# Performance work log

Measured on AMD Instinct MI355X. Metric: run time of the kernel, lower is better.

Reference implementation:

```python
import jax, jax.numpy as jnp
import numpy as np

N, E, G = 100000, 800000, 64
F_IN, H = 92, 4
D1, D2, D3 = 32, 64, 128  # per-head out dims: hidden//2, hidden, 2*hidden
HID, LAT = 64, 128
FINAL = H * D3  # 512
NEG_SLOPE = 0.2


def _p(key, shape, scale=0.05):
    return jax.random.normal(key, shape, dtype=jnp.float32) * scale


def setup_inputs() -> dict:
    key = jax.random.key(0)
    ks = jax.random.split(key, 32)
    node_feat = jax.random.normal(ks[0], (N, F_IN), dtype=jnp.float32)
    src = jax.random.randint(ks[1], (E,), 0, N)
    dst = jax.random.randint(ks[2], (E,), 0, N)
    graph_id = jnp.sort(jax.random.randint(ks[3], (N,), 0, G))
    d = {"node_feat": node_feat, "src": src, "dst": dst, "graph_id": graph_id}
    # GAT layer params (DGL GATConv: fc no bias, attn_l/attn_r [H,D], bias [H*D])
    dims = [(F_IN, D1), (H * D1, D2), (H * D2, D3)]
    i = 4
    for li, (fi, do) in enumerate(dims, 1):
        d[f"W{li}"] = _p(ks[i], (fi, H * do)); i += 1
        d[f"al{li}"] = _p(ks[i], (H, do)); i += 1
        d[f"ar{li}"] = _p(ks[i], (H, do)); i += 1
        d[f"b{li}"] = jnp.zeros((H * do,), dtype=jnp.float32)
    # gate MLP: Linear(final, hid) -> ReLU -> Linear(hid, 1)
    d["Wg1"] = _p(ks[i], (FINAL, HID)); i += 1
    d["bg1"] = jnp.zeros((HID,), dtype=jnp.float32)
    d["Wg2"] = _p(ks[i], (HID, 1)); i += 1
    d["bg2"] = jnp.zeros((1,), dtype=jnp.float32)
    d["Wmu"] = _p(ks[i], (FINAL, LAT)); i += 1
    d["bmu"] = jnp.zeros((LAT,), dtype=jnp.float32)
    d["Wlv"] = _p(ks[i], (FINAL, LAT)); i += 1
    d["blv"] = jnp.zeros((LAT,), dtype=jnp.float32)
    return d


def gat_layer(h, W, al, ar, b, src, dst, heads, d_out):
    n = h.shape[0]
    Wh = (h @ W).reshape(n, heads, d_out)                      # [N,H,D]
    el = jnp.einsum('nhd,hd->nh', Wh, al)                      # a_l . Wh
    er = jnp.einsum('nhd,hd->nh', Wh, ar)
    e = jax.nn.leaky_relu(el[src] + er[dst], NEG_SLOPE)        # [E,H]
    m = jax.ops.segment_max(e, dst, num_segments=n)
    m = jnp.where(jnp.isfinite(m), m, 0.0)                     # zero-in-degree guard
    ex = jnp.exp(e - m[dst])
    s = jax.ops.segment_sum(ex, dst, num_segments=n)
    a = ex / jnp.maximum(s[dst], 1e-9)                         # edge softmax
    msg = a[:, :, None] * Wh[src]                              # [E,H,D] (peak intermediate)
    out = jax.ops.segment_sum(msg, dst, num_segments=n)        # scatter-aggregate
    out = out + b.reshape(1, heads, d_out)
    return out.reshape(n, heads * d_out)                       # flatten(1)


def attention_pool(h, graph_id, Wg1, bg1, Wg2, bg2, num_graphs):
    gate = jax.nn.relu(h @ Wg1 + bg1) @ Wg2 + bg2              # [N,1]
    m = jax.ops.segment_max(gate, graph_id, num_segments=num_graphs)
    ex = jnp.exp(gate - m[graph_id])
    s = jax.ops.segment_sum(ex, graph_id, num_segments=num_graphs)
    a = ex / jnp.maximum(s[graph_id], 1e-9)                    # softmax over nodes per graph
    return jax.ops.segment_sum(a * h, graph_id, num_segments=num_graphs)  # [G,final]


def reference(node_feat, src, dst, graph_id,
              W1, al1, ar1, b1, W2, al2, ar2, b2, W3, al3, ar3, b3,
              Wg1, bg1, Wg2, bg2, Wmu, bmu, Wlv, blv):
    h = jax.nn.elu(gat_layer(node_feat, W1, al1, ar1, b1, src, dst, H, D1))
    h = jax.nn.elu(gat_layer(h, W2, al2, ar2, b2, src, dst, H, D2))
    h = jax.nn.elu(gat_layer(h, W3, al3, ar3, b3, src, dst, H, D3))
    g = attention_pool(h, graph_id, Wg1, bg1, Wg2, bg2, G)
    mu = g @ Wmu + bmu
    logvar = g @ Wlv + blv
    return (mu, logvar)
```

## Files before the change

kernel.cpp:

```cpp
#include <hip/hip_runtime.h>
#include <math.h>

#define NNODES 100000
#define NEDGES 800000
#define NGRAPH 64
#define NHEAD  4
#define FINALD 512
#define HIDG   64
#define LATD   128
#define K1P    96
#define NB_SCAN 98
#define PQ     16

typedef unsigned int uint;
typedef unsigned short ushort;
typedef __attribute__((ext_vector_type(8))) short bf16x8;
typedef __attribute__((ext_vector_type(4))) float f32x4;

__device__ __forceinline__ float bflo(uint u) { return __uint_as_float(u << 16); }
__device__ __forceinline__ float bfhi(uint u) { return __uint_as_float(u & 0xffff0000u); }
__device__ __forceinline__ ushort f2bf(float f) {
    uint u = __float_as_uint(f);
    return (ushort)((u + 0x7fffu + ((u >> 16) & 1u)) >> 16);
}
__device__ __forceinline__ uint pack2(float a, float b) {
    return (uint)f2bf(a) | ((uint)f2bf(b) << 16);
}

__device__ __forceinline__ void async_copy16(const ushort* gsrc, ushort* lds_base) {
    __builtin_amdgcn_global_load_lds(
        (const __attribute__((address_space(1))) uint*)gsrc,
        (__attribute__((address_space(3))) uint*)lds_base,
        16, 0, 0);
}

__global__ void init_kernel(int* __restrict__ deg, const int* __restrict__ gid,
                            int* __restrict__ gstart) {
    int i = blockIdx.x * blockDim.x + threadIdx.x;
    if (i < NNODES) deg[i] = 0;
    if (i <= NGRAPH) {
        int lo = 0, hi = NNODES;
        while (lo < hi) {
            int mid = (lo + hi) >> 1;
            if (gid[mid] < i) lo = mid + 1; else hi = mid;
        }
        gstart[i] = lo;
    }
}
__global__ void count_kernel(const int* __restrict__ dst, int* __restrict__ deg) {
    int e = blockIdx.x * blockDim.x + threadIdx.x;
    if (e < NEDGES) atomicAdd(&deg[dst[e]], 1);
}
__global__ __launch_bounds__(1024) void scan_block_kernel(const int* __restrict__ deg,
                                                          int* __restrict__ off,
                                                          int* __restrict__ bsum) {
    __shared__ int buf[1024];
    int t = threadIdx.x;
    int i = blockIdx.x * 1024 + t;
    int x = (i < NNODES) ? deg[i] : 0;
    buf[t] = x;
    __syncthreads();
    for (int s = 1; s < 1024; s <<= 1) {
        int v = (t >= s) ? buf[t - s] : 0;
        __syncthreads();
        buf[t] += v;
        __syncthreads();
    }
    if (i < NNODES) off[i] = buf[t] - x;
    if (t == 1023) bsum[blockIdx.x] = buf[1023];
}
__global__ __launch_bounds__(128) void scan_bsum_kernel(int* __restrict__ bsum) {
    __shared__ int buf[128];
    int t = threadIdx.x;
    int x = (t < NB_SCAN) ? bsum[t] : 0;
    buf[t] = x;
    __syncthreads();
    for (int s = 1; s < 128; s <<= 1) {
        int v = (t >= s) ? buf[t - s] : 0;
        __syncthreads();
        buf[t] += v;
        __syncthreads();
    }
    if (t < NB_SCAN) bsum[t] = buf[t] - x;
    if (t == 0) bsum[NB_SCAN] = buf[NB_SCAN - 1];
}
__global__ __launch_bounds__(1024) void scan_add_kernel(int* __restrict__ off,
                                                        const int* __restrict__ bsum,
                                                        int* __restrict__ cursor) {
    int i = blockIdx.x * 1024 + threadIdx.x;
    if (i < NNODES) {
        int v = off[i] + bsum[blockIdx.x];
        off[i] = v;
        cursor[i] = v;
    }
    if (i == 0) off[NNODES] = bsum[NB_SCAN];
}
__global__ void scatter_kernel(const int* __restrict__ src, const int* __restrict__ dst,
                               int* __restrict__ cursor, int* __restrict__ src_csr) {
    int e = blockIdx.x * blockDim.x + threadIdx.x;
    if (e >= NEDGES) return;
    int p = atomicAdd(&cursor[dst[e]], 1);
    src_csr[p] = src[e];
}

#define C1 (128 * K1P)
#define C2 (256 * 128)
#define C3 (512 * 256)
#define CG (64 * 512)
#define CX (NNODES * K1P)
#define CTOT (C1 + C2 + C3 + CG + CX + NNODES)
__global__ void conv_all_kernel(const float* __restrict__ W1, const float* __restrict__ W2,
                                const float* __restrict__ W3, const float* __restrict__ Wg1,
                                const float* __restrict__ nf,
                                ushort* __restrict__ Bt1, ushort* __restrict__ Bt2,
                                ushort* __restrict__ Bt3, ushort* __restrict__ Btg,
                                ushort* __restrict__ x0, float* __restrict__ gate) {
    int i = blockIdx.x * blockDim.x + threadIdx.x;
    if (i < C1) {
        int n = i / K1P, k = i - n * K1P;
        Bt1[i] = (k < 92) ? f2bf(W1[(size_t)k * 128 + n]) : (ushort)0;
        return;
    }
    i -= C1;
    if (i < C2) {
        int n = i >> 7, k = i & 127;
        Bt2[i] = f2bf(W2[(size_t)k * 256 + n]);
        return;
    }
    i -= C2;
    if (i < C3) {
        int n = i >> 8, k = i & 255;
        Bt3[i] = f2bf(W3[(size_t)k * 512 + n]);
        return;
    }
    i -= C3;
    if (i < CG) {
        int n = i >> 9, k = i & 511;
        Btg[i] = f2bf(Wg1[(size_t)k * 64 + n]);
        return;
    }
    i -= CG;
    if (i < CX) {
        int n = i / K1P, k = i - n * K1P;
        x0[i] = (k < 92) ? f2bf(nf[(size_t)n * 92 + k]) : (ushort)0;
        return;
    }
    i -= CX;
    if (i < NNODES) gate[i] = 0.f;
}

template <int BN, int MODE>
__global__ __launch_bounds__(256) void mfma_gemm(const ushort* __restrict__ A,
                                                 const ushort* __restrict__ Bt,
                                                 const float* __restrict__ bias,
                                                 ushort* __restrict__ C,
                                                 const float* __restrict__ Wg2,
                                                 float* __restrict__ gate,
                                                 int M, int K, int N) {
    constexpr int WNS = BN / 2;
    constexpr int NT = WNS / 16;
    __shared__ ushort Alds[128][32];
    __shared__ ushort Blds[BN][32];
    int tid = threadIdx.x;
    int wave = tid >> 6, lane = tid & 63;
    int wm = wave & 1, wn = wave >> 1;
    int quad = lane >> 4, l16 = lane & 15;
    int rowBase = blockIdx.y * 128;
    int colBase = blockIdx.x * BN;

    int srow = lane >> 2;
    int scol = (lane & 3) * 8;

    f32x4 acc[4][NT];
#pragma unroll
    for (int i = 0; i < 4; i++)
#pragma unroll
        for (int j = 0; j < NT; j++) acc[i][j] = (f32x4){0.f, 0.f, 0.f, 0.f};

    for (int k0 = 0; k0 < K; k0 += 32) {
#pragma unroll
        for (int c = 0; c < 2; c++) {
            int chunk = wave * 2 + c;
            int row = rowBase + chunk * 16 + srow;
            async_copy16(&A[(size_t)row * K + k0 + scol], &Alds[chunk * 16][0]);
        }
        if constexpr (BN == 128) {
#pragma unroll
            for (int c = 0; c < 2; c++) {
                int chunk = wave * 2 + c;
                int row = colBase + chunk * 16 + srow;
                async_copy16(&Bt[(size_t)row * K + k0 + scol], &Blds[chunk * 16][0]);
            }
        } else {
            int row = colBase + wave * 16 + srow;
            async_copy16(&Bt[(size_t)row * K + k0 + scol], &Blds[wave * 16][0]);
        }
        __syncthreads();
        bf16x8 af[4], bf[NT];
#pragma unroll
        for (int i = 0; i < 4; i++)
            af[i] = *(const bf16x8*)&Alds[wm * 64 + i * 16 + l16][quad * 8];
#pragma unroll
        for (int j = 0; j < NT; j++)
            bf[j] = *(const bf16x8*)&Blds[wn * WNS + j * 16 + l16][quad * 8];
#pragma unroll
        for (int i = 0; i < 4; i++)
#pragma unroll
            for (int j = 0; j < NT; j++)
                acc[i][j] = __builtin_amdgcn_mfma_f32_16x16x32_bf16(af[i], bf[j], acc[i][j], 0, 0, 0);
        __syncthreads();
    }

    if constexpr (MODE == 0) {
#pragma unroll
        for (int i = 0; i < 4; i++) {
#pragma unroll
            for (int j = 0; j < NT; j++) {
                int col = colBase + wn * WNS + j * 16 + l16;
#pragma unroll
                for (int r = 0; r < 4; r++) {
                    int row = rowBase + wm * 64 + i * 16 + quad * 4 + r;
                    if (row < M) C[(size_t)row * N + col] = f2bf(acc[i][j][r]);
                }
            }
        }
    } else {
        float bb[NT], wg[NT];
#pragma unroll
        for (int j = 0; j < NT; j++) {
            int col = colBase + wn * WNS + j * 16 + l16;
            bb[j] = bias[col];
            wg[j] = Wg2[col];
        }
#pragma unroll
        for (int i = 0; i < 4; i++) {
            float pd[4] = {0.f, 0.f, 0.f, 0.f};
#pragma unroll
            for (int j = 0; j < NT; j++) {
#pragma unroll
                for (int r = 0; r < 4; r++) {
                    float x = fmaxf(acc[i][j][r] + bb[j], 0.f);
                    pd[r] = fmaf(x, wg[j], pd[r]);
                }
            }
#pragma unroll
            for (int m = 1; m < 16; m <<= 1)
#pragma unroll
                for (int r = 0; r < 4; r++)
                    pd[r] += __shfl_xor(pd[r], m, 64);
            if (l16 == 0) {
#pragma unroll
                for (int r = 0; r < 4; r++) {
                    int row = rowBase + wm * 64 + i * 16 + quad * 4 + r;
                    if (row < M) atomicAdd(&gate[row], pd[r]);
                }
            }
        }
    }
}

template <int HD>
__global__ __launch_bounds__(256) void eler_node(const ushort* __restrict__ Wh,
                                                 const float* __restrict__ al,
                                                 const float* __restrict__ ar,
                                                 float* __restrict__ el,
                                                 float* __restrict__ er) {
    constexpr int LPN = HD / 8;
    constexpr int NPW = 64 / LPN;
    constexpr int S = (HD / NHEAD) / 8;
    int wave = threadIdx.x >> 6;
    int lane = threadIdx.x & 63;
    int sub = lane & (LPN - 1);
    int n = blockIdx.x * (4 * NPW) + wave * NPW + lane / LPN;
    int d0 = sub * 8;
    uint4 v = *(const uint4*)&Wh[(size_t)n * HD + d0];
    float w0 = bflo(v.x), w1 = bfhi(v.x), w2 = bflo(v.y), w3 = bfhi(v.y);
    float w4 = bflo(v.z), w5 = bfhi(v.z), w6 = bflo(v.w), w7 = bfhi(v.w);
    float4 a0 = *(const float4*)&al[d0];
    float4 a1 = *(const float4*)&al[d0 + 4];
    float4 b0 = *(const float4*)&ar[d0];
    float4 b1 = *(const float4*)&ar[d0 + 4];
    float sl, sr;
    sl = w0 * a0.x; sl = fmaf(w1, a0.y, sl); sl = fmaf(w2, a0.z, sl); sl = fmaf(w3, a0.w, sl);
    sl = fmaf(w4, a1.x, sl); sl = fmaf(w5, a1.y, sl); sl = fmaf(w6, a1.z, sl); sl = fmaf(w7, a1.w, sl);
    sr = w0 * b0.x; sr = fmaf(w1, b0.y, sr); sr = fmaf(w2, b0.z, sr); sr = fmaf(w3, b0.w, sr);
    sr = fmaf(w4, b1.x, sr); sr = fmaf(w5, b1.y, sr); sr = fmaf(w6, b1.z, sr); sr = fmaf(w7, b1.w, sr);
#pragma unroll
    for (int o = S / 2; o > 0; o >>= 1) {
        sl += __shfl_down(sl, o, 64);
        sr += __shfl_down(sr, o, 64);
    }
    if ((sub & (S - 1)) == 0) {
        int h = sub / S;
        el[n * 4 + h] = sl;
        er[n * 4 + h] = sr;
    }
}

__global__ void attn_node(const int* __restrict__ src_csr, const int* __restrict__ off,
                          const float4* __restrict__ el4, const float4* __restrict__ er4,
                          float4* __restrict__ aw4, float4* __restrict__ nsum4) {
    int n = blockIdx.x * blockDim.x + threadIdx.x;
    if (n >= NNODES) return;
    int i0 = off[n], i1 = off[n + 1];
    float4 ern = er4[n];
    float m0 = -1e30f, m1 = -1e30f, m2 = -1e30f, m3 = -1e30f;
    for (int i = i0; i < i1; i += 8) {
        int cnt = i1 - i; if (cnt > 8) cnt = 8;
        int s8[8];
#pragma unroll
        for (int j = 0; j < 8; j++)
            if (j < cnt) s8[j] = src_csr[i + j];
        float4 e8[8];
#pragma unroll
        for (int j = 0; j < 8; j++)
            if (j < cnt) e8[j] = el4[s8[j]];
#pragma unroll
        for (int j = 0; j < 8; j++) {
            if (j < cnt) {
                float4 x = e8[j];
                x.x += ern.x; x.y += ern.y; x.z += ern.z; x.w += ern.w;
                x.x = (x.x >= 0.f) ? x.x : 0.2f * x.x;
                x.y = (x.y >= 0.f) ? x.y : 0.2f * x.y;
                x.z = (x.z >= 0.f) ? x.z : 0.2f * x.z;
                x.w = (x.w >= 0.f) ? x.w : 0.2f * x.w;
                aw4[i + j] = x;
                m0 = fmaxf(m0, x.x); m1 = fmaxf(m1, x.y);
                m2 = fmaxf(m2, x.z); m3 = fmaxf(m3, x.w);
            }
        }
    }
    float4 s = make_float4(0.f, 0.f, 0.f, 0.f);
    for (int i = i0; i < i1; i++) {
        float4 x = aw4[i];
        x.x = expf(x.x - m0); x.y = expf(x.y - m1);
        x.z = expf(x.z - m2); x.w = expf(x.w - m3);
        s.x += x.x; s.y += x.y; s.z += x.z; s.w += x.w;
        aw4[i] = x;
    }
    nsum4[n] = s;
}

__global__ __launch_bounds__(256) void gat_aggregate(const int* __restrict__ src_csr,
                                                     const int* __restrict__ off,
                                                     const ushort* __restrict__ Wh,
                                                     const float* __restrict__ aw,
                                                     const float* __restrict__ nsum,
                                                     const float* __restrict__ bias,
                                                     ushort* __restrict__ out,
                                                     int HD, int logHD8, int logD, int total8) {
    int idx = blockIdx.x * blockDim.x + threadIdx.x;
    if (idx >= total8) return;
    int n = idx >> logHD8;
    int d = (idx & ((1 << logHD8) - 1)) << 3;
    int h = d >> logD;
    int i0 = off[n], i1 = off[n + 1];
    float acc[8] = {0.f, 0.f, 0.f, 0.f, 0.f, 0.f, 0.f, 0.f};
    for (int i = i0; i < i1; i += 8) {
        int cnt = i1 - i; if (cnt > 8) cnt = 8;
        int s8[8]; float w8[8];
#pragma unroll
        for (int j = 0; j < 8; j++) {
            if (j < cnt) {
                s8[j] = src_csr[i + j];
                w8[j] = aw[(i + j) * 4 + h];
            }
        }
#pragma unroll
        for (int j = 0; j < 8; j++) {
            if (j < cnt) {
                uint4 v = *(const uint4*)&Wh[(size_t)s8[j] * HD + d];
                float w = w8[j];
                acc[0] = fmaf(w, bflo(v.x), acc[0]);
                acc[1] = fmaf(w, bfhi(v.x), acc[1]);
                acc[2] = fmaf(w, bflo(v.y), acc[2]);
                acc[3] = fmaf(w, bfhi(v.y), acc[3]);
                acc[4] = fmaf(w, bflo(v.z), acc[4]);
                acc[5] = fmaf(w, bfhi(v.z), acc[5]);
                acc[6] = fmaf(w, bflo(v.w), acc[6]);
                acc[7] = fmaf(w, bfhi(v.w), acc[7]);
            }
        }
    }
    float inv = 1.f / fmaxf(nsum[n * 4 + h], 1e-9f);
    float r[8];
#pragma unroll
    for (int j = 0; j < 8; j++) {
        float x = acc[j] * inv + bias[d + j];
        r[j] = (x > 0.f) ? x : (expf(x) - 1.f);
    }
    uint4 o;
    o.x = pack2(r[0], r[1]);
    o.y = pack2(r[2], r[3]);
    o.z = pack2(r[4], r[5]);
    o.w = pack2(r[6], r[7]);
    *(uint4*)&out[(size_t)n * HD + d] = o;
}

__global__ __launch_bounds__(256) void graph_softmax_kernel(const float* __restrict__ gate,
                                                            const int* __restrict__ gstart,
                                                            float* __restrict__ exn,
                                                            float* __restrict__ gsum) {
    int g = blockIdx.x, t = threadIdx.x;
    int n0 = gstart[g], n1 = gstart[g + 1];
    __shared__ float red[256];
    float m = -1e30f;
    for (int n = n0 + t; n < n1; n += 256) m = fmaxf(m, gate[n]);
    red[t] = m; __syncthreads();
    for (int s = 128; s > 0; s >>= 1) {
        if (t < s) red[t] = fmaxf(red[t], red[t + s]);
        __syncthreads();
    }
    m = red[0]; __syncthreads();
    float sum = 0.f;
    for (int n = n0 + t; n < n1; n += 256) {
        float v = expf(gate[n] - m);
        exn[n] = v;
        sum += v;
    }
    red[t] = sum; __syncthreads();
    for (int s = 128; s > 0; s >>= 1) {
        if (t < s) red[t] += red[t + s];
        __syncthreads();
    }
    if (t == 0) gsum[g] = red[0];
}

__global__ __launch_bounds__(128) void pool_partial(const ushort* __restrict__ h,
                                                    const float* __restrict__ exn,
                                                    const int* __restrict__ gstart,
                                                    float* __restrict__ partial) {
    int g = blockIdx.x, q = blockIdx.y;
    int n0 = gstart[g], n1 = gstart[g + 1];
    int len = n1 - n0;
    int chunk = (len + PQ - 1) / PQ;
    int s = n0 + q * chunk;
    int e = s + chunk; if (e > n1) e = n1;
    int d4 = threadIdx.x;
    const uint2* h2 = (const uint2*)h;
    float a0 = 0.f, a1 = 0.f, a2 = 0.f, a3 = 0.f;
    for (int n = s; n < e; n++) {
        float w = exn[n];
        uint2 v = h2[(size_t)n * 128 + d4];
        a0 = fmaf(w, bflo(v.x), a0);
        a1 = fmaf(w, bfhi(v.x), a1);
        a2 = fmaf(w, bflo(v.y), a2);
        a3 = fmaf(w, bfhi(v.y), a3);
    }
    *(float4*)&partial[((size_t)(g * PQ + q)) * FINALD + d4 * 4] = make_float4(a0, a1, a2, a3);
}

__global__ __launch_bounds__(128) void final_kernel(const float* __restrict__ partial,
                                                    const float* __restrict__ gsum,
                                                    const float* __restrict__ Wmu,
                                                    const float* __restrict__ bmu,
                                                    const float* __restrict__ Wlv,
                                                    const float* __restrict__ blv,
                                                    float* __restrict__ out) {
    int g = blockIdx.x, j = threadIdx.x;
    __shared__ float pooled[FINALD];
    const float* p = partial + (size_t)g * PQ * FINALD;
    for (int k = j; k < FINALD; k += 128) {
        float v = 0.f;
#pragma unroll
        for (int q = 0; q < PQ; q++) v += p[q * FINALD + k];
        pooled[k] = v;
    }
    __syncthreads();
    float am = 0.f, av = 0.f;
    for (int k = 0; k < FINALD; k++) {
        float pv = pooled[k];
        am = fmaf(pv, Wmu[k * LATD + j], am);
        av = fmaf(pv, Wlv[k * LATD + j], av);
    }
    float inv = 1.f / fmaxf(gsum[g], 1e-9f);
    out[g * LATD + j] = am * inv + bmu[j];
    out[NGRAPH * LATD + g * LATD + j] = av * inv + blv[j];
}

extern "C" void kernel_launch(void* const* d_in, const int* in_sizes, int n_in,
                              void* d_out, int out_size, void* d_ws, size_t ws_size,
                              hipStream_t stream) {
    (void)in_sizes; (void)n_in; (void)out_size; (void)ws_size;
    const float* node_feat = (const float*)d_in[0];
    const int* src = (const int*)d_in[1];
    const int* dst = (const int*)d_in[2];
    const int* gid = (const int*)d_in[3];
    const float* W[3]    = {(const float*)d_in[4],  (const float*)d_in[8],  (const float*)d_in[12]};
    const float* al[3]   = {(const float*)d_in[5],  (const float*)d_in[9],  (const float*)d_in[13]};
    const float* ar[3]   = {(const float*)d_in[6],  (const float*)d_in[10], (const float*)d_in[14]};
    const float* bias[3] = {(const float*)d_in[7],  (const float*)d_in[11], (const float*)d_in[15]};
    const float* Wg1 = (const float*)d_in[16];
    const float* bg1 = (const float*)d_in[17];
    const float* Wg2 = (const float*)d_in[18];
    const float* Wmu = (const float*)d_in[20];
    const float* bmu = (const float*)d_in[21];
    const float* Wlv = (const float*)d_in[22];
    const float* blv = (const float*)d_in[23];

    char* ws = (char*)d_ws;
    size_t woff = 0;
    auto carve = [&](size_t bytes) {
        void* p = ws + woff;
        woff = (woff + bytes + 255) & ~(size_t)255;
        return p;
    };
    ushort* hA      = (ushort*)carve((size_t)NNODES * 512 * 2);
    ushort* hB      = (ushort*)carve((size_t)NNODES * 512 * 2);
    float*  el      = (float*) carve((size_t)NNODES * 4 * 4);
    float*  er      = (float*) carve((size_t)NNODES * 4 * 4);
    float*  aw      = (float*) carve((size_t)NEDGES * 4 * 4);
    float*  nsum    = (float*) carve((size_t)NNODES * 4 * 4);
    int*    deg     = (int*)   carve((size_t)NNODES * 4);
    int*    off     = (int*)   carve((size_t)(NNODES + 1) * 4);
    int*    cursor  = (int*)   carve((size_t)NNODES * 4);
    int*    src_csr = (int*)   carve((size_t)NEDGES * 4);
    int*    bsum    = (int*)   carve((size_t)(NB_SCAN + 1) * 4);
    float*  gate    = (float*) carve((size_t)NNODES * 4);
    float*  exn     = (float*) carve((size_t)NNODES * 4);
    int*    gstart  = (int*)   carve((size_t)(NGRAPH + 1) * 4);
    float*  partial = (float*) carve((size_t)NGRAPH * PQ * FINALD * 4);
    float*  gsum    = (float*) carve((size_t)NGRAPH * 4);
    ushort* Bt1     = (ushort*)carve((size_t)128 * K1P * 2);
    ushort* Bt2     = (ushort*)carve((size_t)256 * 128 * 2);
    ushort* Bt3     = (ushort*)carve((size_t)512 * 256 * 2);
    ushort* Btg     = (ushort*)carve((size_t)64 * 512 * 2 + 4096);
    ushort* x0      = hA;

    init_kernel<<<(NNODES + 255) / 256, 256, 0, stream>>>(deg, gid, gstart);
    count_kernel<<<(NEDGES + 255) / 256, 256, 0, stream>>>(dst, deg);
    scan_block_kernel<<<NB_SCAN, 1024, 0, stream>>>(deg, off, bsum);
    scan_bsum_kernel<<<1, 128, 0, stream>>>(bsum);
    scan_add_kernel<<<NB_SCAN, 1024, 0, stream>>>(off, bsum, cursor);
    scatter_kernel<<<(NEDGES + 255) / 256, 256, 0, stream>>>(src, dst, cursor, src_csr);
    conv_all_kernel<<<(CTOT + 255) / 256, 256, 0, stream>>>(
        W[0], W[1], W[2], Wg1, node_feat, Bt1, Bt2, Bt3, Btg, x0, gate);

    const int HDs[3]    = {128, 256, 512};
    const int logHD8[3] = {4, 5, 6};
    const int logD[3]   = {5, 6, 7};
    const int MB = (NNODES + 127) / 128;

    for (int l = 0; l < 3; l++) {
        int HD = HDs[l];
        if (l == 0)
            mfma_gemm<128, 0><<<dim3(1, MB), 256, 0, stream>>>(
                x0, Bt1, nullptr, hB, nullptr, nullptr, NNODES, K1P, 128);
        else if (l == 1)
            mfma_gemm<128, 0><<<dim3(2, MB), 256, 0, stream>>>(
                hA, Bt2, nullptr, hB, nullptr, nullptr, NNODES, 128, 256);
        else
            mfma_gemm<128, 0><<<dim3(4, MB), 256, 0, stream>>>(
                hA, Bt3, nullptr, hB, nullptr, nullptr, NNODES, 256, 512);
        if (l == 0)      eler_node<128><<<NNODES / 16, 256, 0, stream>>>(hB, al[l], ar[l], el, er);
        else if (l == 1) eler_node<256><<<NNODES / 8, 256, 0, stream>>>(hB, al[l], ar[l], el, er);
        else             eler_node<512><<<NNODES / 4, 256, 0, stream>>>(hB, al[l], ar[l], el, er);
        attn_node<<<(NNODES + 255) / 256, 256, 0, stream>>>(
            src_csr, off, (const float4*)el, (const float4*)er, (float4*)aw, (float4*)nsum);
        int total8 = NNODES * (HD / 8);
        gat_aggregate<<<(total8 + 255) / 256, 256, 0, stream>>>(
            src_csr, off, hB, aw, nsum, bias[l], hA, HD, logHD8[l], logD[l], total8);
    }

    mfma_gemm<64, 1><<<dim3(1, MB), 256, 0, stream>>>(
        hA, Btg, bg1, nullptr, Wg2, gate, NNODES, FINALD, HIDG);
    graph_softmax_kernel<<<NGRAPH, 256, 0, stream>>>(gate, gstart, exn, gsum);
    pool_partial<<<dim3(NGRAPH, PQ), 128, 0, stream>>>(hA, exn, gstart, partial);
    final_kernel<<<NGRAPH, 128, 0, stream>>>(partial, gsum, Wmu, bmu, Wlv, blv, (float*)d_out);
}
```

Measured before the change: 775.9 us.

## Map one wavefront per destination node in GAT aggregation with scalar edge indices

Replaces the per-thread aggregation, where each thread owned 8 feature columns of a node, with a wavefront-per-node kernel. Lanes split the feature row, and source indices and edge offsets are made wave-uniform through readfirstlane, so gathers from one source row are contiguous across the wave. For the 512-wide layer the row is covered in two launches. The aim is to cut divergent per-thread edge loops and redundant index loads and to improve gather coalescing, at the cost of narrower per-lane loads and repeated edge-list traversal across the layer-3 passes.

```diff
diff --git a/kernel.cpp b/kernel.cpp
--- a/kernel.cpp
+++ b/kernel.cpp
@@ -25,6 +25,10 @@
 }
 __device__ __forceinline__ uint pack2(float a, float b) {
     return (uint)f2bf(a) | ((uint)f2bf(b) << 16);
+}
+__device__ __forceinline__ void fmabf2(float w, uint v, float& a0, float& a1) {
+    a0 = fmaf(w, bflo(v), a0);
+    a1 = fmaf(w, bfhi(v), a1);
 }
 
 __device__ __forceinline__ void async_copy16(const ushort* gsrc, ushort* lds_base) {
@@ -341,60 +345,86 @@
     nsum4[n] = s;
 }
 
-__global__ __launch_bounds__(256) void gat_aggregate(const int* __restrict__ src_csr,
-                                                     const int* __restrict__ off,
-                                                     const ushort* __restrict__ Wh,
-                                                     const float* __restrict__ aw,
-                                                     const float* __restrict__ nsum,
-                                                     const float* __restrict__ bias,
-                                                     ushort* __restrict__ out,
-                                                     int HD, int logHD8, int logD, int total8) {
-    int idx = blockIdx.x * blockDim.x + threadIdx.x;
-    if (idx >= total8) return;
-    int n = idx >> logHD8;
-    int d = (idx & ((1 << logHD8) - 1)) << 3;
-    int h = d >> logD;
-    int i0 = off[n], i1 = off[n + 1];
-    float acc[8] = {0.f, 0.f, 0.f, 0.f, 0.f, 0.f, 0.f, 0.f};
-    for (int i = i0; i < i1; i += 8) {
-        int cnt = i1 - i; if (cnt > 8) cnt = 8;
-        int s8[8]; float w8[8];
-#pragma unroll
-        for (int j = 0; j < 8; j++) {
-            if (j < cnt) {
-                s8[j] = src_csr[i + j];
-                w8[j] = aw[(i + j) * 4 + h];
-            }
-        }
-#pragma unroll
-        for (int j = 0; j < 8; j++) {
-            if (j < cnt) {
-                uint4 v = *(const uint4*)&Wh[(size_t)s8[j] * HD + d];
-                float w = w8[j];
-                acc[0] = fmaf(w, bflo(v.x), acc[0]);
-                acc[1] = fmaf(w, bfhi(v.x), acc[1]);
-                acc[2] = fmaf(w, bflo(v.y), acc[2]);
-                acc[3] = fmaf(w, bfhi(v.y), acc[3]);
-                acc[4] = fmaf(w, bflo(v.z), acc[4]);
-                acc[5] = fmaf(w, bfhi(v.z), acc[5]);
-                acc[6] = fmaf(w, bflo(v.w), acc[6]);
-                acc[7] = fmaf(w, bfhi(v.w), acc[7]);
-            }
-        }
-    }
-    float inv = 1.f / fmaxf(nsum[n * 4 + h], 1e-9f);
-    float r[8];
-#pragma unroll
-    for (int j = 0; j < 8; j++) {
-        float x = acc[j] * inv + bias[d + j];
-        r[j] = (x > 0.f) ? x : (expf(x) - 1.f);
-    }
-    uint4 o;
-    o.x = pack2(r[0], r[1]);
-    o.y = pack2(r[2], r[3]);
-    o.z = pack2(r[4], r[5]);
-    o.w = pack2(r[6], r[7]);
-    *(uint4*)&out[(size_t)n * HD + d] = o;
+template <int HD, int DPL>
+__global__ __launch_bounds__(256) void gat_aggregate2(const int* __restrict__ src_csr,
+                                                      const int* __restrict__ off,
+                                                      const ushort* __restrict__ Wh,
+                                                      const float* __restrict__ aw,
+                                                      const float* __restrict__ nsum,
+                                                      const float* __restrict__ bias,
+                                                      ushort* __restrict__ out,
+                                                      int pass) {
+    constexpr int LOGD = (HD == 128) ? 5 : (HD == 256) ? 6 : 7;
+    const int lane = threadIdx.x & 63;
+    const int wv = __builtin_amdgcn_readfirstlane((int)(threadIdx.x >> 6));
+    const int n = blockIdx.x * 4 + wv;
+    const int d = pass * (64 * DPL) + lane * DPL;
+    const int h = d >> LOGD;
+    const int i0 = __builtin_amdgcn_readfirstlane(off[n]);
+    const int i1 = __builtin_amdgcn_readfirstlane(off[n + 1]);
+
+    float a0 = 0.f, a1 = 0.f, a2 = 0.f, a3 = 0.f;
+    const ushort* __restrict__ col = Wh + d;
+
+    int i = i0;
+    for (; i + 4 <= i1; i += 4) {
+        const int s0 = __builtin_amdgcn_readfirstlane(src_csr[i + 0]);
+        const int s1 = __builtin_amdgcn_readfirstlane(src_csr[i + 1]);
+        const int s2 = __builtin_amdgcn_readfirstlane(src_csr[i + 2]);
+        const int s3 = __builtin_amdgcn_readfirstlane(src_csr[i + 3]);
+        const float w0 = aw[(i + 0) * 4 + h];
+        const float w1 = aw[(i + 1) * 4 + h];
+        const float w2 = aw[(i + 2) * 4 + h];
+        const float w3 = aw[(i + 3) * 4 + h];
+        if constexpr (DPL == 4) {
+            uint2 v0 = *(const uint2*)&col[(size_t)s0 * HD];
+            uint2 v1 = *(const uint2*)&col[(size_t)s1 * HD];
+            uint2 v2 = *(const uint2*)&col[(size_t)s2 * HD];
+            uint2 v3 = *(const uint2*)&col[(size_t)s3 * HD];
+            fmabf2(w0, v0.x, a0, a1); fmabf2(w0, v0.y, a2, a3);
+            fmabf2(w1, v1.x, a0, a1); fmabf2(w1, v1.y, a2, a3);
+            fmabf2(w2, v2.x, a0, a1); fmabf2(w2, v2.y, a2, a3);
+            fmabf2(w3, v3.x, a0, a1); fmabf2(w3, v3.y, a2, a3);
+        } else {
+            uint v0 = *(const uint*)&col[(size_t)s0 * HD];
+            uint v1 = *(const uint*)&col[(size_t)s1 * HD];
+            uint v2 = *(const uint*)&col[(size_t)s2 * HD];
+            uint v3 = *(const uint*)&col[(size_t)s3 * HD];
+            fmabf2(w0, v0, a0, a1);
+            fmabf2(w1, v1, a0, a1);
+            fmabf2(w2, v2, a0, a1);
+            fmabf2(w3, v3, a0, a1);
+        }
+    }
+    for (; i < i1; ++i) {
+        const int s0 = __builtin_amdgcn_readfirstlane(src_csr[i]);
+        const float w0 = aw[i * 4 + h];
+        if constexpr (DPL == 4) {
+            uint2 v0 = *(const uint2*)&col[(size_t)s0 * HD];
+            fmabf2(w0, v0.x, a0, a1); fmabf2(w0, v0.y, a2, a3);
+        } else {
+            uint v0 = *(const uint*)&col[(size_t)s0 * HD];
+            fmabf2(w0, v0, a0, a1);
+        }
+    }
+
+    const float inv = 1.f / fmaxf(nsum[n * 4 + h], 1e-9f);
+    float x0 = a0 * inv + bias[d + 0];
+    float x1 = a1 * inv + bias[d + 1];
+    x0 = (x0 > 0.f) ? x0 : (expf(x0) - 1.f);
+    x1 = (x1 > 0.f) ? x1 : (expf(x1) - 1.f);
+    if constexpr (DPL == 4) {
+        float x2 = a2 * inv + bias[d + 2];
+        float x3 = a3 * inv + bias[d + 3];
+        x2 = (x2 > 0.f) ? x2 : (expf(x2) - 1.f);
+        x3 = (x3 > 0.f) ? x3 : (expf(x3) - 1.f);
+        uint2 o;
+        o.x = pack2(x0, x1);
+        o.y = pack2(x2, x3);
+        *(uint2*)&out[(size_t)n * HD + d] = o;
+    } else {
+        *(uint*)&out[(size_t)n * HD + d] = pack2(x0, x1);
+    }
 }
 
 __global__ __launch_bounds__(256) void graph_softmax_kernel(const float* __restrict__ gate,
@@ -536,31 +566,34 @@
     conv_all_kernel<<<(CTOT + 255) / 256, 256, 0, stream>>>(
         W[0], W[1], W[2], Wg1, node_feat, Bt1, Bt2, Bt3, Btg, x0, gate);
 
-    const int HDs[3]    = {128, 256, 512};
-    const int logHD8[3] = {4, 5, 6};
-    const int logD[3]   = {5, 6, 7};
     const int MB = (NNODES + 127) / 128;
-
-    for (int l = 0; l < 3; l++) {
-        int HD = HDs[l];
-        if (l == 0)
-            mfma_gemm<128, 0><<<dim3(1, MB), 256, 0, stream>>>(
-                x0, Bt1, nullptr, hB, nullptr, nullptr, NNODES, K1P, 128);
-        else if (l == 1)
-            mfma_gemm<128, 0><<<dim3(2, MB), 256, 0, stream>>>(
-                hA, Bt2, nullptr, hB, nullptr, nullptr, NNODES, 128, 256);
-        else
-            mfma_gemm<128, 0><<<dim3(4, MB), 256, 0, stream>>>(
-                hA, Bt3, nullptr, hB, nullptr, nullptr, NNODES, 256, 512);
-        if (l == 0)      eler_node<128><<<NNODES / 16, 256, 0, stream>>>(hB, al[l], ar[l], el, er);
-        else if (l == 1) eler_node<256><<<NNODES / 8, 256, 0, stream>>>(hB, al[l], ar[l], el, er);
-        else             eler_node<512><<<NNODES / 4, 256, 0, stream>>>(hB, al[l], ar[l], el, er);
-        attn_node<<<(NNODES + 255) / 256, 256, 0, stream>>>(
-            src_csr, off, (const float4*)el, (const float4*)er, (float4*)aw, (float4*)nsum);
-        int total8 = NNODES * (HD / 8);
-        gat_aggregate<<<(total8 + 255) / 256, 256, 0, stream>>>(
-            src_csr, off, hB, aw, nsum, bias[l], hA, HD, logHD8[l], logD[l], total8);
-    }
+    const int AGB = NNODES / 4;
+
+    mfma_gemm<128, 0><<<dim3(1, MB), 256, 0, stream>>>(
+        x0, Bt1, nullptr, hB, nullptr, nullptr, NNODES, K1P, 128);
+    eler_node<128><<<NNODES / 16, 256, 0, stream>>>(hB, al[0], ar[0], el, er);
+    attn_node<<<(NNODES + 255) / 256, 256, 0, stream>>>(
+        src_csr, off, (const float4*)el, (const float4*)er, (float4*)aw, (float4*)nsum);
+    gat_aggregate2<128, 2><<<AGB, 256, 0, stream>>>(
+        src_csr, off, hB, aw, nsum, bias[0], hA, 0);
+
+    mfma_gemm<128, 0><<<dim3(2, MB), 256, 0, stream>>>(
+        hA, Bt2, nullptr, hB, nullptr, nullptr, NNODES, 128, 256);
+    eler_node<256><<<NNODES / 8, 256, 0, stream>>>(hB, al[1], ar[1], el, er);
+    attn_node<<<(NNODES + 255) / 256, 256, 0, stream>>>(
+        src_csr, off, (const float4*)el, (const float4*)er, (float4*)aw, (float4*)nsum);
+    gat_aggregate2<256, 4><<<AGB, 256, 0, stream>>>(
+        src_csr, off, hB, aw, nsum, bias[1], hA, 0);
+
+    mfma_gemm<128, 0><<<dim3(4, MB), 256, 0, stream>>>(
+        hA, Bt3, nullptr, hB, nullptr, nullptr, NNODES, 256, 512);
+    eler_node<512><<<NNODES / 4, 256, 0, stream>>>(hB, al[2], ar[2], el, er);
+    attn_node<<<(NNODES + 255) / 256, 256, 0, stream>>>(
+        src_csr, off, (const float4*)el, (const float4*)er, (float4*)aw, (float4*)nsum);
+    gat_aggregate2<512, 4><<<AGB, 256, 0, stream>>>(
+        src_csr, off, hB, aw, nsum, bias[2], hA, 0);
+    gat_aggregate2<512, 4><<<AGB, 256, 0, stream>>>(
+        src_csr, off, hB, aw, nsum, bias[2], hA, 1);
 
     mfma_gemm<64, 1><<<dim3(1, MB), 256, 0, stream>>>(
         hA, Btg, bg1, nullptr, Wg2, gate, NNODES, FINALD, HIDG);
```

New measurement: 771.0 us. About the same (-0.6%).
